# Optimization experiments

Hardware: AMD Instinct MI355X
Metric: run time of the kernel (lower is better)

The kernel has to match this reference:

```python
import jax, jax.numpy as jnp
import numpy as np

BATCH, SEQ, D_MODEL = 2, 4096, 1024
D_STATE, EXPAND = 64, 2
D_INNER = D_MODEL * EXPAND


def setup_inputs() -> dict:
    key = jax.random.key(0)
    ks = jax.random.split(key, 12)
    s = 0.02
    return {
        "x": jax.random.normal(ks[0], (BATCH, SEQ, D_MODEL), dtype=jnp.float32),
        "W_in": jax.random.normal(ks[1], (D_MODEL, 2 * D_INNER), dtype=jnp.float32) * s,
        "b_in": jnp.zeros((2 * D_INNER,), dtype=jnp.float32),
        "W_xp": jax.random.normal(ks[2], (D_INNER, D_STATE), dtype=jnp.float32) * s,
        "b_xp": jnp.zeros((D_STATE,), dtype=jnp.float32),
        "W_dt": jax.random.normal(ks[3], (D_INNER, D_MODEL), dtype=jnp.float32) * s,
        "b_dt": jnp.zeros((D_MODEL,), dtype=jnp.float32),
        "W_out": jax.random.normal(ks[4], (D_INNER, D_MODEL), dtype=jnp.float32) * s,
        "b_out": jnp.zeros((D_MODEL,), dtype=jnp.float32),
        "A_log": jax.random.normal(ks[5], (D_STATE,), dtype=jnp.float32),
        "D": jax.random.normal(ks[6], (D_MODEL,), dtype=jnp.float32),
    }


def _silu(v):
    return v * jax.nn.sigmoid(v)


def reference(x, W_in, b_in, W_xp, b_xp, W_dt, b_dt, W_out, b_out, A_log, D):
    # in_proj -> split into inner stream and residual gate
    xr = x @ W_in + b_in                       # [B,S,2*d_inner]
    x_inner, res = jnp.split(xr, 2, axis=-1)   # each [B,S,d_inner]
    x_inner = _silu(x_inner)

    A = -jnp.exp(A_log)                        # [N]
    delta = jax.nn.softplus(x_inner @ W_dt + b_dt)  # [B,S,d_model]
    mean_delta = delta.mean(axis=-1)           # [B,S] (scalar dt per step, as in source)
    a = jnp.exp(A[None, None, :] * mean_delta[..., None])  # [B,S,N] discrete A
    bx = x_inner @ W_xp + b_xp                 # [B,S,N] input injection

    # sequential selective-scan recurrence: state = a_t * state + bx_t
    def step(state, inp):
        a_t, bx_t = inp                        # [B,N] each
        state = a_t * state + bx_t
        return state, state.sum(axis=-1)       # emit per-batch scalar

    init = jnp.zeros((x.shape[0], D_STATE), dtype=x.dtype)
    _, s_sum = jax.lax.scan(step, init, (a.transpose(1, 0, 2), bx.transpose(1, 0, 2)))
    s_sum = s_sum.T                            # [B,S]

    y = s_sum[..., None] * x_inner             # [B,S,d_inner]
    y = y * _silu(res)
    out = y @ W_out + b_out + x * D
    return out
```

## Files before the change

### kernel.cpp

```cpp
#include <hip/hip_runtime.h>

#define SEQ 4096
#define DMODEL 1024
#define DSTATE 64
#define DINNER 2048
#define MROWS 8192
#define NCAT 1152
#define NCHUNK 64
#define LCHUNK 64

typedef __attribute__((ext_vector_type(8))) __bf16 bf16x8;
typedef __attribute__((ext_vector_type(8))) short short8;
typedef __attribute__((ext_vector_type(4))) float floatx4;

__device__ inline float bf2f(short s) {
  union { unsigned u; float f; } c;
  c.u = ((unsigned)(unsigned short)s) << 16;
  return c.f;
}
__device__ inline short f2bf(float f) {
  union { float f; unsigned u; } c; c.f = f;
  unsigned r = 0x7fffu + ((c.u >> 16) & 1u);
  return (short)((c.u + r) >> 16);
}
__device__ inline float silu_f(float v) {
  return v * __builtin_amdgcn_rcpf(1.f + __expf(-v));
}
__device__ inline float softplus_f(float v) {
  return fmaxf(v, 0.f) + log1pf(__expf(-fabsf(v)));
}
__device__ inline void gld_lds16(const void* g, void* l) {
  __builtin_amdgcn_global_load_lds(
      (__attribute__((address_space(1))) void*)g,
      (__attribute__((address_space(3))) void*)l, 16, 0, 0);
}

__device__ inline size_t permOff(int r, int k, int K) {
  return (((size_t)(r >> 4) * (K >> 3) + (k >> 3)) << 7) + ((r & 15) << 3) + (k & 7);
}

#define PP0 4096
#define PP1 (PP0 + 4096)
#define PP2 (PP1 + 2048)
#define PP3 (PP2 + 128)
#define PP4 (PP3 + 2048)

__device__ void tile_transpose_perm(const float* __restrict__ in, short* __restrict__ out,
                                    int R, int C, int bx, int by, float (*tile)[33]) {
  const int tx = threadIdx.x & 31, ty = threadIdx.x >> 5;
  const int cb = bx * 32, rb = by * 32;
#pragma unroll
  for (int i = 0; i < 32; i += 8) {
    int r = rb + ty + i, c = cb + tx;
    tile[ty + i][tx] = (r < R && c < C) ? in[(size_t)r * C + c] : 0.f;
  }
  __syncthreads();
#pragma unroll
  for (int i = 0; i < 32; i += 8) {
    int orow = cb + ty + i, oc = rb + tx;
    if (orow < C && oc < R) out[permOff(orow, oc, R)] = f2bf(tile[tx][ty + i]);
  }
}

__global__ void prepass_kernel(const float* __restrict__ x, short* __restrict__ x_bf,
                               const float* __restrict__ W_in, short* __restrict__ Wt_in,
                               const float* __restrict__ W_dt, const float* __restrict__ W_xp,
                               short* __restrict__ Bcat,
                               const float* __restrict__ W_out, short* __restrict__ Wt_out) {
  __shared__ float tile[32][33];
  const int blk = blockIdx.x;
  if (blk < PP0) {
    int o = blk * 256 + threadIdx.x;
    int m = o & 15, rest = o >> 4;
    int c = rest & 127, p = rest >> 7;
    const float* src = x + ((size_t)(p * 16 + m)) * 1024 + c * 8;
    float4 v0 = ((const float4*)src)[0];
    float4 v1 = ((const float4*)src)[1];
    short8 ov;
    ov[0] = f2bf(v0.x); ov[1] = f2bf(v0.y); ov[2] = f2bf(v0.z); ov[3] = f2bf(v0.w);
    ov[4] = f2bf(v1.x); ov[5] = f2bf(v1.y); ov[6] = f2bf(v1.z); ov[7] = f2bf(v1.w);
    ((short8*)x_bf)[o] = ov;
  } else if (blk < PP1) {
    int t = blk - PP0;
    tile_transpose_perm(W_in, Wt_in, 1024, 4096, t & 127, t >> 7, tile);
  } else if (blk < PP2) {
    int t = blk - PP1;
    tile_transpose_perm(W_dt, Bcat, 2048, 1024, t & 31, t >> 5, tile);
  } else if (blk < PP3) {
    int t = blk - PP2;
    tile_transpose_perm(W_xp, Bcat + (size_t)1024 * DINNER, 2048, 64, t & 1, t >> 1, tile);
  } else {
    int t = blk - PP3;
    tile_transpose_perm(W_out, Wt_out, 2048, 1024, t & 31, t >> 5, tile);
  }
}

template <int MODE, int KTOT, int KSL, int NT, int ZS>
__global__ __launch_bounds__(512, 2) void gemm256(
    const short* __restrict__ A, const short* __restrict__ Bt,
    const float* __restrict__ bias,
    void* __restrict__ out0, void* __restrict__ out1)
{
  __shared__ __attribute__((aligned(16))) short sLds[65536];

  const int tid = threadIdx.x;
  const int lane = tid & 63;
  const int w = tid >> 6;
  const int wr = w >> 2, wc = w & 3;
  const int m = lane & 15, quad = lane >> 4;

  const int xcd = blockIdx.x & 7;
  const int q = blockIdx.x >> 3;
  const int mt = xcd * 4 + (q & 3);
  const int rest = q >> 2;
  const int ntile = rest % NT;
  const int z = rest / NT;
  const int bM = mt * 256, bN = ntile * 256;
  const int kbeg = z * KSL;

  floatx4 acc[8][4] = {};

  const size_t PS = (size_t)KTOT * 16;
  const short* AgA = A  + ((size_t)(bM >> 4) + w) * PS + (size_t)kbeg * 16 + lane * 8;
  const short* AgB = AgA + 8 * PS;
  const short* BgA = Bt + ((size_t)(bN >> 4) + w) * PS + (size_t)kbeg * 16 + lane * 8;
  const short* BgB = BgA + 8 * PS;

  constexpr int KT = KSL / 64;

  auto STAGE_Q = [&](int t, int qq) {
    const size_t go = (size_t)t * 1024 + (size_t)(qq >> 1) * 512;
    short* d = sLds + ((t & 1) << 15) + ((qq & 1) << 14) + ((qq >> 1) << 13) + w * 512;
    const short* g0 = (qq & 1) ? BgA : AgA;
    const short* g1 = (qq & 1) ? BgB : AgB;
    gld_lds16(g0 + go, d);
    gld_lds16(g1 + go, d + 4096);
  };

  const int aoff = wr * 4096 + quad * 128 + m * 8;
  const int boff = 16384 + wc * 2048 + quad * 128 + m * 8;

  bf16x8 aA[4], aB[4], bA[4], bB[4];

  STAGE_Q(0, 0); STAGE_Q(0, 1); STAGE_Q(0, 2); STAGE_Q(0, 3);
  asm volatile("s_waitcnt vmcnt(4)" ::: "memory");
  asm volatile("s_barrier" ::: "memory");
  {
    const short* bs = sLds;
#pragma unroll
    for (int rt = 0; rt < 4; ++rt) aA[rt] = *(const bf16x8*)(bs + aoff + rt * 512);
#pragma unroll
    for (int ct = 0; ct < 4; ++ct) bA[ct] = *(const bf16x8*)(bs + boff + ct * 512);
    if (KT > 1) STAGE_Q(1, 0);
    __builtin_amdgcn_sched_barrier(0);
  }

#pragma unroll 1
  for (int t = 0; t < KT; ++t) {
    const short* bs = sLds + ((t & 1) << 15);
    const bool pf = (t + 1 < KT);

#pragma unroll
    for (int rt = 0; rt < 4; ++rt) aB[rt] = *(const bf16x8*)(bs + aoff + (4 + rt) * 512);
    if (pf) {
      STAGE_Q(t + 1, 1);
      asm volatile("s_waitcnt vmcnt(4)" ::: "memory");
    } else {
      asm volatile("s_waitcnt vmcnt(0)" ::: "memory");
    }
    __builtin_amdgcn_sched_barrier(0);
    __builtin_amdgcn_s_setprio(1);
#pragma unroll
    for (int rt = 0; rt < 4; ++rt)
#pragma unroll
      for (int ct = 0; ct < 4; ++ct)
        acc[rt][ct] = __builtin_amdgcn_mfma_f32_16x16x32_bf16(aA[rt], bA[ct], acc[rt][ct], 0, 0, 0);
    __builtin_amdgcn_s_setprio(0);
    __builtin_amdgcn_sched_barrier(0);

    asm volatile("s_waitcnt lgkmcnt(0)" ::: "memory");
    asm volatile("s_barrier" ::: "memory");
#pragma unroll
    for (int rt = 0; rt < 4; ++rt) aA[rt] = *(const bf16x8*)(bs + 8192 + aoff + rt * 512);
#pragma unroll
    for (int ct = 0; ct < 4; ++ct) bB[ct] = *(const bf16x8*)(bs + 8192 + boff + ct * 512);
    if (pf) STAGE_Q(t + 1, 2);
    __builtin_amdgcn_sched_barrier(0);
    __builtin_amdgcn_s_setprio(1);
#pragma unroll
    for (int rt = 0; rt < 4; ++rt)
#pragma unroll
      for (int ct = 0; ct < 4; ++ct)
        acc[4 + rt][ct] = __builtin_amdgcn_mfma_f32_16x16x32_bf16(aB[rt], bA[ct], acc[4 + rt][ct], 0, 0, 0);
    __builtin_amdgcn_s_setprio(0);
    __builtin_amdgcn_sched_barrier(0);

#pragma unroll
    for (int rt = 0; rt < 4; ++rt) aB[rt] = *(const bf16x8*)(bs + 8192 + aoff + (4 + rt) * 512);
    if (pf) {
      STAGE_Q(t + 1, 3);
      asm volatile("s_waitcnt vmcnt(4)" ::: "memory");
    }
    __builtin_amdgcn_sched_barrier(0);
    __builtin_amdgcn_s_setprio(1);
#pragma unroll
    for (int rt = 0; rt < 4; ++rt)
#pragma unroll
      for (int ct = 0; ct < 4; ++ct)
        acc[rt][ct] = __builtin_amdgcn_mfma_f32_16x16x32_bf16(aA[rt], bB[ct], acc[rt][ct], 0, 0, 0);
    __builtin_amdgcn_s_setprio(0);
    __builtin_amdgcn_sched_barrier(0);

    if (pf) {
      asm volatile("s_waitcnt lgkmcnt(0)" ::: "memory");
      asm volatile("s_barrier" ::: "memory");
      const short* bs2 = sLds + (((t + 1) & 1) << 15);
#pragma unroll
      for (int rt = 0; rt < 4; ++rt) aA[rt] = *(const bf16x8*)(bs2 + aoff + rt * 512);
#pragma unroll
      for (int ct = 0; ct < 4; ++ct) bA[ct] = *(const bf16x8*)(bs2 + boff + ct * 512);
      if (t + 2 < KT) STAGE_Q(t + 2, 0);
      __builtin_amdgcn_sched_barrier(0);
    }
    __builtin_amdgcn_s_setprio(1);
#pragma unroll
    for (int rt = 0; rt < 4; ++rt)
#pragma unroll
      for (int ct = 0; ct < 4; ++ct)
        acc[4 + rt][ct] = __builtin_amdgcn_mfma_f32_16x16x32_bf16(aB[rt], bB[ct], acc[4 + rt][ct], 0, 0, 0);
    __builtin_amdgcn_s_setprio(0);
    __builtin_amdgcn_sched_barrier(0);
  }

  const int rowbase = bM + wr * 128;
  const int colbase = bN + wc * 64;

  if constexpr (MODE == 0) {
    short* dst = (bN < DINNER) ? (short*)out0 : (short*)out1;
    const int cb = (bN < DINNER) ? colbase : colbase - DINNER;
#pragma unroll
    for (int rt = 0; rt < 8; ++rt) {
      const size_t rowPan = ((size_t)(rowbase >> 4) + rt) << 8;
#pragma unroll
      for (int ct = 0; ct < 4; ++ct) {
        const int colA = colbase + ct * 16 + m;
        const int colP = cb + ct * 16 + m;
        const size_t base = ((rowPan + (colP >> 3)) << 7) + (colP & 7) + ((size_t)quad * 32);
        const float bv = bias[colA];
#pragma unroll
        for (int reg = 0; reg < 4; ++reg) {
          float val = acc[rt][ct][reg] + bv;
          dst[base + reg * 8] = f2bf(silu_f(val));
        }
      }
    }
  } else {
    constexpr int N = NT * 256;
    short* dst = (short*)out0 + (size_t)z * MROWS * N;
#pragma unroll
    for (int rt = 0; rt < 8; ++rt)
#pragma unroll
      for (int ct = 0; ct < 4; ++ct) {
        const int col = colbase + ct * 16 + m;
#pragma unroll
        for (int reg = 0; reg < 4; ++reg) {
          const int r = rowbase + rt * 16 + quad * 4 + reg;
          dst[(size_t)r * N + col] = f2bf(acc[rt][ct][reg]);
        }
      }
  }
}

__global__ __launch_bounds__(256) void xp_gemm(const short* __restrict__ xi,
                                               const short* __restrict__ Bxp,
                                               float* __restrict__ bxp) {
  __shared__ __attribute__((aligned(16))) short sA[2][4096];
  __shared__ __attribute__((aligned(16))) short sB[2][4096];
  const int tid = threadIdx.x, lane = tid & 63, w = tid >> 6;
  const int m = lane & 15, quad = lane >> 4;
  const int z = blockIdx.x >> 7;
  const int rb = (blockIdx.x & 127) * 64;
  const size_t PS = (size_t)2048 * 16;
  const short* Ag = xi  + ((size_t)(rb >> 4) + w) * PS + (size_t)z * 1024 * 16 + lane * 8;
  const short* Bg = Bxp + (size_t)w * PS + (size_t)z * 1024 * 16 + lane * 8;
  floatx4 acc[4] = {};
  auto STAGE = [&](int t) {
    const size_t go = (size_t)t * 1024;
    short* da = sA[t & 1] + w * 1024;
    short* db = sB[t & 1] + w * 1024;
    gld_lds16(Ag + go, da); gld_lds16(Ag + go + 512, da + 512);
    gld_lds16(Bg + go, db); gld_lds16(Bg + go + 512, db + 512);
  };
  STAGE(0);
#pragma unroll 1
  for (int t = 0; t < 16; ++t) {
    __builtin_amdgcn_s_barrier();
    if (t + 1 < 16) {
      STAGE(t + 1);
      asm volatile("s_waitcnt vmcnt(4)" ::: "memory");
    } else {
      asm volatile("s_waitcnt vmcnt(0)" ::: "memory");
    }
    __builtin_amdgcn_s_barrier();
    const short* a0 = sA[t & 1] + w * 1024 + quad * 128 + m * 8;
    const short* b0 = sB[t & 1] + quad * 128 + m * 8;
#pragma unroll
    for (int kh = 0; kh < 2; ++kh) {
      bf16x8 a = *(const bf16x8*)(a0 + kh * 512);
#pragma unroll
      for (int ct = 0; ct < 4; ++ct) {
        bf16x8 b = *(const bf16x8*)(b0 + ct * 1024 + kh * 512);
        acc[ct] = __builtin_amdgcn_mfma_f32_16x16x32_bf16(a, b, acc[ct], 0, 0, 0);
      }
    }
  }
  float* dst = bxp + (size_t)z * MROWS * DSTATE;
#pragma unroll
  for (int ct = 0; ct < 4; ++ct)
#pragma unroll
    for (int reg = 0; reg < 4; ++reg)
      dst[(size_t)(rb + w * 16 + quad * 4 + reg) * DSTATE + ct * 16 + m] = acc[ct][reg];
}

__global__ void g2_epilogue(const short* __restrict__ p, const float* __restrict__ b_dt,
                            float* __restrict__ md_sum) {
  const int row = blockIdx.x * 4 + (threadIdx.x >> 6);
  const int lane = threadIdx.x & 63;
  const size_t base0 = (size_t)row * 1024;
  const size_t base1 = base0 + (size_t)MROWS * 1024;
  short8 a0 = *(const short8*)(p + base0 + lane * 16);
  short8 a1 = *(const short8*)(p + base0 + lane * 16 + 8);
  short8 c0 = *(const short8*)(p + base1 + lane * 16);
  short8 c1 = *(const short8*)(p + base1 + lane * 16 + 8);
  float s = 0.f;
#pragma unroll
  for (int j = 0; j < 8; ++j) {
    s += softplus_f(bf2f(a0[j]) + bf2f(c0[j]) + b_dt[lane * 16 + j]);
    s += softplus_f(bf2f(a1[j]) + bf2f(c1[j]) + b_dt[lane * 16 + 8 + j]);
  }
  s += __shfl_xor(s, 1);  s += __shfl_xor(s, 2);  s += __shfl_xor(s, 4);
  s += __shfl_xor(s, 8);  s += __shfl_xor(s, 16); s += __shfl_xor(s, 32);
  if (lane == 0) md_sum[row] = s;
}

__global__ void g4_epilogue(const short* __restrict__ p, const float* __restrict__ b_out,
                            const float* __restrict__ x, const float* __restrict__ Dv,
                            float* __restrict__ out) {
  const int r = blockIdx.x, c = threadIdx.x * 4;
  const size_t o = (size_t)r * DMODEL + c;
  short4 a0 = *(const short4*)(p + o);
  short4 a1 = *(const short4*)(p + (size_t)MROWS * DMODEL + o);
  float4 xv = *(const float4*)(x + o);
  float4 ov;
  ov.x = bf2f(a0.x) + bf2f(a1.x) + b_out[c + 0] + xv.x * Dv[c + 0];
  ov.y = bf2f(a0.y) + bf2f(a1.y) + b_out[c + 1] + xv.y * Dv[c + 1];
  ov.z = bf2f(a0.z) + bf2f(a1.z) + b_out[c + 2] + xv.z * Dv[c + 2];
  ov.w = bf2f(a0.w) + bf2f(a1.w) + b_out[c + 3] + xv.w * Dv[c + 3];
  *(float4*)(out + o) = ov;
}

__global__ void scan_phase1(const float* __restrict__ md_sum, const float* __restrict__ A_log,
                            const float* __restrict__ bxp, const float* __restrict__ b_xp,
                            float* __restrict__ chunk_prod, float* __restrict__ chunk_end) {
  const int n = threadIdx.x;
  const int c = blockIdx.x & (NCHUNK - 1);
  const int b = blockIdx.x >> 6;
  const float An = -__expf(A_log[n]);
  const float bxn = b_xp[n];
  const float* bx0 = bxp;
  const float* bx1 = bxp + (size_t)MROWS * DSTATE;
  float prod = 1.f, st = 0.f;
  const int t0 = c * LCHUNK;
#pragma unroll 4
  for (int i = 0; i < LCHUNK; ++i) {
    const int t = t0 + i;
    const float md = md_sum[b * SEQ + t] * (1.f / DMODEL);
    const float a = __expf(An * md);
    const size_t idx = ((size_t)(b * SEQ + t)) * DSTATE + n;
    st = a * st + (bx0[idx] + bx1[idx] + bxn);
    prod *= a;
  }
  chunk_prod[(b * NCHUNK + c) * DSTATE + n] = prod;
  chunk_end [(b * NCHUNK + c) * DSTATE + n] = st;
}

__global__ void scan_phase3(const float* __restrict__ md_sum, const float* __restrict__ A_log,
                            const float* __restrict__ bxp, const float* __restrict__ b_xp,
                            const float* __restrict__ chunk_prod,
                            const float* __restrict__ chunk_end,
                            float* __restrict__ s_sum) {
  const int n = threadIdx.x;
  const int c = blockIdx.x & (NCHUNK - 1);
  const int b = blockIdx.x >> 6;
  const float An = -__expf(A_log[n]);
  const float bxn = b_xp[n];
  const float* bx0 = bxp;
  const float* bx1 = bxp + (size_t)MROWS * DSTATE;
  float st = 0.f;
#pragma unroll 4
  for (int cc = 0; cc < c; ++cc) {
    const size_t idx = ((size_t)(b * NCHUNK + cc)) * DSTATE + n;
    st = chunk_prod[idx] * st + chunk_end[idx];
  }
  const int t0 = c * LCHUNK;
#pragma unroll 4
  for (int i = 0; i < LCHUNK; ++i) {
    const int t = t0 + i;
    const float md = md_sum[b * SEQ + t] * (1.f / DMODEL);
    const float a = __expf(An * md);
    const size_t idx = ((size_t)(b * SEQ + t)) * DSTATE + n;
    st = a * st + (bx0[idx] + bx1[idx] + bxn);
    float v = st;
    v += __shfl_xor(v, 32); v += __shfl_xor(v, 16); v += __shfl_xor(v, 8);
    v += __shfl_xor(v, 4);  v += __shfl_xor(v, 2);  v += __shfl_xor(v, 1);
    if (n == 0) s_sum[b * SEQ + t] = v;
  }
}

__global__ void ymul_kernel(const short* __restrict__ xi, const short* __restrict__ g,
                            const float* __restrict__ s_sum, short* __restrict__ y) {
  const int o = blockIdx.x * 256 + threadIdx.x;
  const int row = ((o >> 12) << 4) | (o & 15);
  const size_t base = (size_t)o * 8;
  const float s = s_sum[row];
  short8 xv = *(const short8*)(xi + base);
  short8 gv = *(const short8*)(g + base);
  short8 yv;
#pragma unroll
  for (int k = 0; k < 8; ++k) yv[k] = f2bf(s * bf2f(xv[k]) * bf2f(gv[k]));
  *(short8*)(y + base) = yv;
}

extern "C" void kernel_launch(void* const* d_in, const int* in_sizes, int n_in,
                              void* d_out, int out_size, void* d_ws, size_t ws_size,
                              hipStream_t stream) {
  const float* x     = (const float*)d_in[0];
  const float* W_in  = (const float*)d_in[1];
  const float* b_in  = (const float*)d_in[2];
  const float* W_xp  = (const float*)d_in[3];
  const float* b_xp  = (const float*)d_in[4];
  const float* W_dt  = (const float*)d_in[5];
  const float* b_dt  = (const float*)d_in[6];
  const float* W_out = (const float*)d_in[7];
  const float* b_out = (const float*)d_in[8];
  const float* A_log = (const float*)d_in[9];
  const float* Dv    = (const float*)d_in[10];

  char* ws = (char*)d_ws;
  size_t off = 0;
  auto alloc = [&](size_t bytes) -> void* {
    void* p = (void*)(ws + off);
    off += (bytes + 255) & ~(size_t)255;
    return p;
  };
  short* x_bf    = (short*)alloc((size_t)MROWS * DMODEL * 2);
  short* Wt_in   = (short*)alloc((size_t)4096 * 1024 * 2);
  short* Bcat    = (short*)alloc((size_t)NCAT * DINNER * 2);
  short* Wt_out  = (short*)alloc((size_t)1024 * 2048 * 2);
  short* xi      = (short*)alloc((size_t)MROWS * DINNER * 2);
  short* gbuf    = (short*)alloc((size_t)MROWS * DINNER * 2);
  short* ybuf    = (short*)alloc((size_t)MROWS * DINNER * 2);
  short* p2      = (short*)alloc((size_t)2 * MROWS * 1024 * 2);
  float* md_sum  = (float*)alloc((size_t)MROWS * 4);
  float* bxp     = (float*)alloc((size_t)2 * MROWS * DSTATE * 4);
  float* cprod   = (float*)alloc((size_t)2 * NCHUNK * DSTATE * 4);
  float* cend    = (float*)alloc((size_t)2 * NCHUNK * DSTATE * 4);
  float* s_sum   = (float*)alloc((size_t)MROWS * 4);

  prepass_kernel<<<PP4, 256, 0, stream>>>(x, x_bf, W_in, Wt_in, W_dt, W_xp, Bcat, W_out, Wt_out);

  gemm256<0, 1024, 1024, 16, 1><<<512, 512, 0, stream>>>(x_bf, Wt_in, b_in, xi, gbuf);
  gemm256<1, 2048, 1024, 4, 2><<<256, 512, 0, stream>>>(xi, Bcat, nullptr, p2, nullptr);
  xp_gemm<<<256, 256, 0, stream>>>(xi, Bcat + (size_t)1024 * DINNER, bxp);
  g2_epilogue<<<MROWS / 4, 256, 0, stream>>>(p2, b_dt, md_sum);
  scan_phase1<<<2 * NCHUNK, DSTATE, 0, stream>>>(md_sum, A_log, bxp, b_xp, cprod, cend);
  scan_phase3<<<2 * NCHUNK, DSTATE, 0, stream>>>(md_sum, A_log, bxp, b_xp, cprod, cend, s_sum);
  ymul_kernel<<<MROWS * DINNER / 8 / 256, 256, 0, stream>>>(xi, gbuf, s_sum, ybuf);
  gemm256<1, 2048, 1024, 4, 2><<<256, 512, 0, stream>>>(ybuf, Wt_out, nullptr, xi, nullptr);
  g4_epilogue<<<MROWS, 256, 0, stream>>>(xi, b_out, x, Dv, (float*)d_out);
}
```

Measured before the change: 376.1 us.

## Interleave in_proj columns to fuse gate product and defer scan scale to epilogue

Reorders W_in's transposed rows so each GEMM tile holds matching x_inner and residual columns. The in_proj epilogue can then write silu(x_inner) and the product silu(x_inner)*silu(res) directly. Because the per-row scan sum s is a scalar, it is applied after the out-projection in the final epilogue rather than before it. This removes the ymul kernel and one full MROWS×DINNER buffer round trip. The cost is that the bf16 product is now rounded before scaling, which slightly changes numerics.

```diff
diff --git a/kernel.cpp b/kernel.cpp
--- a/kernel.cpp
+++ b/kernel.cpp
@@ -39,6 +39,11 @@
   return (((size_t)(r >> 4) * (K >> 3) + (k >> 3)) << 7) + ((r & 15) << 3) + (k & 7);
 }
 
+__device__ inline int inproj_remap(int oc) {
+  const int c = (oc < DINNER) ? oc : oc - DINNER;
+  return ((c >> 4) << 5) | ((oc < DINNER) ? 0 : 16) | (c & 15);
+}
+
 #define PP0 4096
 #define PP1 (PP0 + 4096)
 #define PP2 (PP1 + 2048)
@@ -46,7 +51,8 @@
 #define PP4 (PP3 + 2048)
 
 __device__ void tile_transpose_perm(const float* __restrict__ in, short* __restrict__ out,
-                                    int R, int C, int bx, int by, float (*tile)[33]) {
+                                    int R, int C, int bx, int by, float (*tile)[33],
+                                    int remap) {
   const int tx = threadIdx.x & 31, ty = threadIdx.x >> 5;
   const int cb = bx * 32, rb = by * 32;
 #pragma unroll
@@ -58,7 +64,10 @@
 #pragma unroll
   for (int i = 0; i < 32; i += 8) {
     int orow = cb + ty + i, oc = rb + tx;
-    if (orow < C && oc < R) out[permOff(orow, oc, R)] = f2bf(tile[tx][ty + i]);
+    if (orow < C && oc < R) {
+      int nr = remap ? inproj_remap(orow) : orow;
+      out[permOff(nr, oc, R)] = f2bf(tile[tx][ty + i]);
+    }
   }
 }
 
@@ -82,16 +91,16 @@
     ((short8*)x_bf)[o] = ov;
   } else if (blk < PP1) {
     int t = blk - PP0;
-    tile_transpose_perm(W_in, Wt_in, 1024, 4096, t & 127, t >> 7, tile);
+    tile_transpose_perm(W_in, Wt_in, 1024, 4096, t & 127, t >> 7, tile, 1);
   } else if (blk < PP2) {
     int t = blk - PP1;
-    tile_transpose_perm(W_dt, Bcat, 2048, 1024, t & 31, t >> 5, tile);
+    tile_transpose_perm(W_dt, Bcat, 2048, 1024, t & 31, t >> 5, tile, 0);
   } else if (blk < PP3) {
     int t = blk - PP2;
-    tile_transpose_perm(W_xp, Bcat + (size_t)1024 * DINNER, 2048, 64, t & 1, t >> 1, tile);
+    tile_transpose_perm(W_xp, Bcat + (size_t)1024 * DINNER, 2048, 64, t & 1, t >> 1, tile, 0);
   } else {
     int t = blk - PP3;
-    tile_transpose_perm(W_out, Wt_out, 2048, 1024, t & 31, t >> 5, tile);
+    tile_transpose_perm(W_out, Wt_out, 2048, 1024, t & 31, t >> 5, tile, 0);
   }
 }
 
@@ -236,21 +245,24 @@
   const int colbase = bN + wc * 64;
 
   if constexpr (MODE == 0) {
-    short* dst = (bN < DINNER) ? (short*)out0 : (short*)out1;
-    const int cb = (bN < DINNER) ? colbase : colbase - DINNER;
-#pragma unroll
-    for (int rt = 0; rt < 8; ++rt) {
-      const size_t rowPan = ((size_t)(rowbase >> 4) + rt) << 8;
-#pragma unroll
-      for (int ct = 0; ct < 4; ++ct) {
-        const int colA = colbase + ct * 16 + m;
-        const int colP = cb + ct * 16 + m;
-        const size_t base = ((rowPan + (colP >> 3)) << 7) + (colP & 7) + ((size_t)quad * 32);
-        const float bv = bias[colA];
+    short* xid = (short*)out0;
+    short* prd = (short*)out1;
+#pragma unroll
+    for (int cp = 0; cp < 2; ++cp) {
+      const int newcolE = colbase + cp * 32 + m;
+      const int phi = ((newcolE >> 5) << 4) | (newcolE & 15);
+      const float bxi = bias[phi];
+      const float bg  = bias[DINNER + phi];
+#pragma unroll
+      for (int rt = 0; rt < 8; ++rt) {
+        const size_t rowPan = ((size_t)(rowbase >> 4) + rt) << 8;
+        const size_t base = ((rowPan + (phi >> 3)) << 7) + (phi & 7) + ((size_t)quad * 32);
 #pragma unroll
         for (int reg = 0; reg < 4; ++reg) {
-          float val = acc[rt][ct][reg] + bv;
-          dst[base + reg * 8] = f2bf(silu_f(val));
+          const float xv = silu_f(acc[rt][2 * cp][reg] + bxi);
+          const float gv = silu_f(acc[rt][2 * cp + 1][reg] + bg);
+          xid[base + reg * 8] = f2bf(xv);
+          prd[base + reg * 8] = f2bf(xv * gv);
         }
       }
     }
@@ -345,17 +357,18 @@
 
 __global__ void g4_epilogue(const short* __restrict__ p, const float* __restrict__ b_out,
                             const float* __restrict__ x, const float* __restrict__ Dv,
-                            float* __restrict__ out) {
+                            const float* __restrict__ s_sum, float* __restrict__ out) {
   const int r = blockIdx.x, c = threadIdx.x * 4;
+  const float s = s_sum[r];
   const size_t o = (size_t)r * DMODEL + c;
   short4 a0 = *(const short4*)(p + o);
   short4 a1 = *(const short4*)(p + (size_t)MROWS * DMODEL + o);
   float4 xv = *(const float4*)(x + o);
   float4 ov;
-  ov.x = bf2f(a0.x) + bf2f(a1.x) + b_out[c + 0] + xv.x * Dv[c + 0];
-  ov.y = bf2f(a0.y) + bf2f(a1.y) + b_out[c + 1] + xv.y * Dv[c + 1];
-  ov.z = bf2f(a0.z) + bf2f(a1.z) + b_out[c + 2] + xv.z * Dv[c + 2];
-  ov.w = bf2f(a0.w) + bf2f(a1.w) + b_out[c + 3] + xv.w * Dv[c + 3];
+  ov.x = s * (bf2f(a0.x) + bf2f(a1.x)) + b_out[c + 0] + xv.x * Dv[c + 0];
+  ov.y = s * (bf2f(a0.y) + bf2f(a1.y)) + b_out[c + 1] + xv.y * Dv[c + 1];
+  ov.z = s * (bf2f(a0.z) + bf2f(a1.z)) + b_out[c + 2] + xv.z * Dv[c + 2];
+  ov.w = s * (bf2f(a0.w) + bf2f(a1.w)) + b_out[c + 3] + xv.w * Dv[c + 3];
   *(float4*)(out + o) = ov;
 }
 
@@ -417,20 +430,6 @@
   }
 }
 
-__global__ void ymul_kernel(const short* __restrict__ xi, const short* __restrict__ g,
-                            const float* __restrict__ s_sum, short* __restrict__ y) {
-  const int o = blockIdx.x * 256 + threadIdx.x;
-  const int row = ((o >> 12) << 4) | (o & 15);
-  const size_t base = (size_t)o * 8;
-  const float s = s_sum[row];
-  short8 xv = *(const short8*)(xi + base);
-  short8 gv = *(const short8*)(g + base);
-  short8 yv;
-#pragma unroll
-  for (int k = 0; k < 8; ++k) yv[k] = f2bf(s * bf2f(xv[k]) * bf2f(gv[k]));
-  *(short8*)(y + base) = yv;
-}
-
 extern "C" void kernel_launch(void* const* d_in, const int* in_sizes, int n_in,
                               void* d_out, int out_size, void* d_ws, size_t ws_size,
                               hipStream_t stream) {
@@ -458,8 +457,7 @@
   short* Bcat    = (short*)alloc((size_t)NCAT * DINNER * 2);
   short* Wt_out  = (short*)alloc((size_t)1024 * 2048 * 2);
   short* xi      = (short*)alloc((size_t)MROWS * DINNER * 2);
-  short* gbuf    = (short*)alloc((size_t)MROWS * DINNER * 2);
-  short* ybuf    = (short*)alloc((size_t)MROWS * DINNER * 2);
+  short* prod    = (short*)alloc((size_t)MROWS * DINNER * 2);
   short* p2      = (short*)alloc((size_t)2 * MROWS * 1024 * 2);
   float* md_sum  = (float*)alloc((size_t)MROWS * 4);
   float* bxp     = (float*)alloc((size_t)2 * MROWS * DSTATE * 4);
@@ -469,13 +467,12 @@
 
   prepass_kernel<<<PP4, 256, 0, stream>>>(x, x_bf, W_in, Wt_in, W_dt, W_xp, Bcat, W_out, Wt_out);
 
-  gemm256<0, 1024, 1024, 16, 1><<<512, 512, 0, stream>>>(x_bf, Wt_in, b_in, xi, gbuf);
+  gemm256<0, 1024, 1024, 16, 1><<<512, 512, 0, stream>>>(x_bf, Wt_in, b_in, xi, prod);
   gemm256<1, 2048, 1024, 4, 2><<<256, 512, 0, stream>>>(xi, Bcat, nullptr, p2, nullptr);
   xp_gemm<<<256, 256, 0, stream>>>(xi, Bcat + (size_t)1024 * DINNER, bxp);
   g2_epilogue<<<MROWS / 4, 256, 0, stream>>>(p2, b_dt, md_sum);
   scan_phase1<<<2 * NCHUNK, DSTATE, 0, stream>>>(md_sum, A_log, bxp, b_xp, cprod, cend);
   scan_phase3<<<2 * NCHUNK, DSTATE, 0, stream>>>(md_sum, A_log, bxp, b_xp, cprod, cend, s_sum);
-  ymul_kernel<<<MROWS * DINNER / 8 / 256, 256, 0, stream>>>(xi, gbuf, s_sum, ybuf);
-  gemm256<1, 2048, 1024, 4, 2><<<256, 512, 0, stream>>>(ybuf, Wt_out, nullptr, xi, nullptr);
-  g4_epilogue<<<MROWS, 256, 0, stream>>>(xi, b_out, x, Dv, (float*)d_out);
-}
+  gemm256<1, 2048, 1024, 4, 2><<<256, 512, 0, stream>>>(prod, Wt_out, nullptr, xi, nullptr);
+  g4_epilogue<<<MROWS, 256, 0, stream>>>(xi, b_out, x, Dv, s_sum, (float*)d_out);
+}
```

After: 354.5 us. 5.7% less time.
